# Optimization experiments

Hardware: AMD Instinct MI355X
Metric: run time of the kernel (lower is better)

Reference implementation:

```python
import jax, jax.numpy as jnp
import numpy as np

NUM_HEADS = 8
HEAD_DIM = 64
EMBED = NUM_HEADS * HEAD_DIM  # 512


def setup_inputs() -> dict:
    key = jax.random.key(0)
    ks = jax.random.split(key, 8)
    B, S = 4, 2048
    s = 1.0 / np.sqrt(HEAD_DIM)
    so = 1.0 / np.sqrt(EMBED)
    return {
        "queries": jax.random.normal(ks[0], (B, S, EMBED), jnp.float32),
        "keys": jax.random.normal(ks[1], (B, S, EMBED), jnp.float32),
        "values": jax.random.normal(ks[2], (B, S, EMBED), jnp.float32),
        "Wq": jax.random.uniform(ks[3], (HEAD_DIM, HEAD_DIM), jnp.float32, -s, s),
        "Wk": jax.random.uniform(ks[4], (HEAD_DIM, HEAD_DIM), jnp.float32, -s, s),
        "Wv": jax.random.uniform(ks[5], (HEAD_DIM, HEAD_DIM), jnp.float32, -s, s),
        "Wo": jax.random.uniform(ks[6], (EMBED, EMBED), jnp.float32, -so, so),
        "bo": jax.random.uniform(ks[7], (EMBED,), jnp.float32, -so, so),
    }


def reference(queries, keys, values, Wq, Wk, Wv, Wo, bo):
    B, Sq, _ = queries.shape
    # Faithful to source: keys/values are (buggily) reshaped from `queries`;
    # with equal seq lens this means k/v come from the queries tensor.
    q = queries.reshape(B, Sq, NUM_HEADS, HEAD_DIM)
    k = q
    v = q
    # per-head linear: torch Linear(x) = x @ W.T
    q = jnp.einsum('bshd,ed->bshe', q, Wq)
    k = jnp.einsum('bshd,ed->bshe', k, Wk)
    v = jnp.einsum('bshd,ed->bshe', v, Wv)
    sim = jnp.einsum('bqhd,bkhd->bhqk', q, k)  # [B,H,Sq,Sk]
    attn = jax.nn.softmax(sim * (1.0 / np.sqrt(HEAD_DIM)), axis=-1)
    out = jnp.einsum('bhqk,bkhd->bqhd', attn, v)
    out = out.reshape(B, Sq, EMBED)
    return out @ Wo.T + bo
```

## Files before the change

### kernel.cpp

```cpp
#include <hip/hip_runtime.h>
#include <cstddef>

#define S_ 2048
#define E_ 512
#define SPLIT_STRIDE 4194304u

typedef __attribute__((ext_vector_type(8)))  short bf16x8;
typedef __attribute__((ext_vector_type(16))) float f32x16;

__device__ __forceinline__ unsigned short f2bf(float f) {
    union { float f; unsigned u; } v; v.f = f;
    return (unsigned short)((v.u + 0x7FFFu + ((v.u >> 16) & 1u)) >> 16);
}
__device__ __forceinline__ unsigned pk2bf(float a, float b) {
    union { float f; unsigned u; } x, y; x.f = a; y.f = b;
    return __builtin_amdgcn_perm(y.u + 0x8000u, x.u + 0x8000u, 0x07060302u);
}
__device__ __forceinline__ float bflo(unsigned u) {
    union { unsigned u; float f; } v; v.u = u << 16; return v.f;
}
__device__ __forceinline__ float bfhi(unsigned u) {
    union { unsigned u; float f; } v; v.u = u & 0xffff0000u; return v.f;
}
__device__ __forceinline__ float fexp2(float x) {
#if __has_builtin(__builtin_amdgcn_exp2f)
    return __builtin_amdgcn_exp2f(x);
#else
    return exp2f(x);
#endif
}

__global__ __launch_bounds__(256) void prep_all(const float* __restrict__ X,
                                                const float* __restrict__ Wq,
                                                const float* __restrict__ Wk,
                                                const float* __restrict__ Wo,
                                                const float* __restrict__ Wv,
                                                unsigned short* __restrict__ Xbf,
                                                unsigned short* __restrict__ XTg,
                                                unsigned short* __restrict__ GT,
                                                unsigned short* __restrict__ W2) {
    __shared__ unsigned short T[64][72];
    const int bi = blockIdx.x, tid = threadIdx.x;
    if (bi < 1024) {
        const int st = bi & 31, h = (bi >> 5) & 7, b = bi >> 8;
        const int s0 = st * 64;
        const int j = tid >> 2, g = tid & 3;
        const float* src = X + ((size_t)(b * S_ + s0 + j) * E_) + h * 64 + g * 16;
        unsigned short us[16];
#pragma unroll
        for (int i = 0; i < 16; i += 4) {
            float4 f = *(const float4*)(src + i);
            us[i] = f2bf(f.x); us[i + 1] = f2bf(f.y);
            us[i + 2] = f2bf(f.z); us[i + 3] = f2bf(f.w);
        }
        size_t xb = ((size_t)(b * S_ + s0 + j) * E_) + h * 64 + g * 16;
        *(uint4*)&Xbf[xb]     = *(uint4*)&us[0];
        *(uint4*)&Xbf[xb + 8] = *(uint4*)&us[8];
#pragma unroll
        for (int i = 0; i < 16; ++i) T[g * 16 + i][j] = us[i];
        __syncthreads();
        const int d = tid >> 2;
        const int pm[16] = {0,1,2,3,8,9,10,11,4,5,6,7,12,13,14,15};
        unsigned short o[16];
#pragma unroll
        for (int i = 0; i < 16; ++i) o[i] = T[d][g * 16 + pm[i]];
        size_t tb = ((size_t)((b * 8 + h) * 64 + d)) * S_ + s0 + g * 16;
        *(uint4*)&XTg[tb]     = *(uint4*)&o[0];
        *(uint4*)&XTg[tb + 8] = *(uint4*)&o[8];
    } else if (bi < 1040) {
        int idx = (bi - 1024) * 256 + tid;
        int c = idx >> 6, d = idx & 63;
        float acc = 0.f;
#pragma unroll 8
        for (int e = 0; e < 64; ++e) acc += Wq[e * 64 + d] * Wk[e * 64 + c];
        GT[c * 64 + d] = f2bf(acc * 0.18033688011112042f);
    } else {
        int idx = (bi - 1040) * 256 + tid;
        int e = idx >> 9, f = idx & 511;
        int h = f >> 6, c = f & 63;
        const float* wo = Wo + e * 512 + h * 64;
        float acc = 0.f;
#pragma unroll 8
        for (int d = 0; d < 64; ++d) acc += wo[d] * Wv[d * 64 + c];
        W2[idx] = f2bf(acc);
    }
}

__global__ __launch_bounds__(128, 2) void attn_mfma(const unsigned short* __restrict__ Xbf,
                                                    const unsigned short* __restrict__ XTg,
                                                    const unsigned short* __restrict__ GT,
                                                    unsigned short* __restrict__ AOp,
                                                    float* __restrict__ Lp) {
    __shared__ union SM {
        unsigned short Q[128][72];
        unsigned short cbuf[2][2 * 64 * 72];
        unsigned short AOt[128][72];
    } sm;

    const int tid = threadIdx.x;
    const int w = tid >> 6, lane = tid & 63;
    const int lm = lane & 31, lh = lane >> 5;
    const int h = blockIdx.x & 7;
    const int rest = blockIdx.x >> 3;
    const int qt = rest & 15, b = (rest >> 4) & 3, split = rest >> 6;
    const int s0 = qt * 128, sk0 = split * (S_ / 2);

    {
        const int r = tid >> 1, c = (tid & 1) * 32;
#pragma unroll
        for (int p = 0; p < 2; ++p) {
            const unsigned short* src = Xbf + ((size_t)(b * S_ + s0 + 64 * p + r)) * E_ + h * 64 + c;
#pragma unroll
            for (int u = 0; u < 4; ++u)
                *(uint4*)&sm.Q[64 * p + r][c + u * 8] = *(const uint4*)(src + u * 8);
        }
    }
    __syncthreads();

    const int rr = tid >> 1, cc = (tid & 1) * 32;
    const unsigned short* srcX = Xbf + ((size_t)(b * S_ + rr)) * E_ + h * 64 + cc;
    const unsigned short* srcT = XTg + ((size_t)((b * 8 + h) * 64 + rr)) * S_ + cc;
    const int ldsOff = rr * 72 + cc;

    uint4 pre[8];
    {
        const unsigned short* sx = srcX + (size_t)sk0 * E_;
        const unsigned short* st = srcT + sk0;
#pragma unroll
        for (int u = 0; u < 4; ++u) pre[u]     = *(const uint4*)(sx + u * 8);
#pragma unroll
        for (int u = 0; u < 4; ++u) pre[4 + u] = *(const uint4*)(st + u * 8);
    }

    bf16x8 Ufrag[2][4];
    {
        f32x16 ua[2][2];
#pragma unroll
        for (int mt = 0; mt < 2; ++mt)
#pragma unroll
            for (int nt = 0; nt < 2; ++nt)
#pragma unroll
                for (int i = 0; i < 16; ++i) ua[mt][nt][i] = 0.f;
#pragma unroll
        for (int ks = 0; ks < 4; ++ks) {
            bf16x8 bG0 = *(const bf16x8*)&GT[(lm +  0) * 64 + ks * 16 + lh * 8];
            bf16x8 bG1 = *(const bf16x8*)&GT[(lm + 32) * 64 + ks * 16 + lh * 8];
#pragma unroll
            for (int mt = 0; mt < 2; ++mt) {
                bf16x8 aQ = *(const bf16x8*)&sm.Q[64 * w + 32 * mt + lm][ks * 16 + lh * 8];
                ua[mt][0] = __builtin_amdgcn_mfma_f32_32x32x16_bf16(aQ, bG0, ua[mt][0], 0, 0, 0);
                ua[mt][1] = __builtin_amdgcn_mfma_f32_32x32x16_bf16(aQ, bG1, ua[mt][1], 0, 0, 0);
            }
        }
#pragma unroll
        for (int mt = 0; mt < 2; ++mt)
#pragma unroll
            for (int nt = 0; nt < 2; ++nt)
#pragma unroll
                for (int r = 0; r < 16; ++r)
                    sm.Q[64 * w + 32 * mt + (r & 3) + 8 * (r >> 2) + 4 * lh][lm + 32 * nt] =
                        f2bf(ua[mt][nt][r]);
#pragma unroll
        for (int g = 0; g < 2; ++g)
#pragma unroll
            for (int ks = 0; ks < 4; ++ks)
                Ufrag[g][ks] = *(const bf16x8*)&sm.Q[64 * w + 32 * g + lm][ks * 16 + lh * 8];
    }
    __syncthreads();

    unsigned short* bufR = sm.cbuf[0];
    unsigned short* bufW = sm.cbuf[1];

    {
#pragma unroll
        for (int u = 0; u < 4; ++u) *(uint4*)(bufR + ldsOff + u * 8)           = pre[u];
#pragma unroll
        for (int u = 0; u < 4; ++u) *(uint4*)(bufR + 64 * 72 + ldsOff + u * 8) = pre[4 + u];
    }
    __syncthreads();

    float lsum0 = 0.f, lsum1 = 0.f;
    f32x16 AO[2][2];
#pragma unroll
    for (int mt = 0; mt < 2; ++mt)
#pragma unroll
        for (int nt = 0; nt < 2; ++nt)
#pragma unroll
            for (int i = 0; i < 16; ++i) AO[mt][nt][i] = 0.f;

    for (int ck = 0; ck < 16; ++ck) {
        const bool have = (ck < 15);
        if (have) {
            const unsigned short* sx = srcX + (size_t)(sk0 + (ck + 1) * 64) * E_;
            const unsigned short* st = srcT + sk0 + (ck + 1) * 64;
#pragma unroll
            for (int u = 0; u < 4; ++u) pre[u]     = *(const uint4*)(sx + u * 8);
#pragma unroll
            for (int u = 0; u < 4; ++u) pre[4 + u] = *(const uint4*)(st + u * 8);
        }

        f32x16 sc[2][2];
#pragma unroll
        for (int mt = 0; mt < 2; ++mt)
#pragma unroll
            for (int nt = 0; nt < 2; ++nt)
#pragma unroll
                for (int i = 0; i < 16; ++i) sc[mt][nt][i] = 0.f;
        __builtin_amdgcn_s_setprio(1);
#pragma unroll
        for (int ks = 0; ks < 4; ++ks)
#pragma unroll
            for (int mt = 0; mt < 2; ++mt) {
                bf16x8 aX = *(const bf16x8*)(bufR + (32 * mt + lm) * 72 + ks * 16 + lh * 8);
                sc[mt][0] = __builtin_amdgcn_mfma_f32_32x32x16_bf16(aX, Ufrag[0][ks], sc[mt][0], 0, 0, 0);
                sc[mt][1] = __builtin_amdgcn_mfma_f32_32x32x16_bf16(aX, Ufrag[1][ks], sc[mt][1], 0, 0, 0);
            }
        __builtin_amdgcn_s_setprio(0);

#pragma unroll
        for (int js = 0; js < 4; ++js) {
            const int mt = js >> 1;
            union { unsigned u[4]; bf16x8 v; } bP0, bP1;
#pragma unroll
            for (int i = 0; i < 4; ++i) {
                const int qq = 2 * (js & 1) + (i >> 1);
                float pa = fexp2(sc[mt][0][qq * 4 + 2 * (i & 1)]);
                float pb = fexp2(sc[mt][0][qq * 4 + 2 * (i & 1) + 1]);
                lsum0 += pa + pb;
                bP0.u[i] = pk2bf(pa, pb);
                float pc = fexp2(sc[mt][1][qq * 4 + 2 * (i & 1)]);
                float pd = fexp2(sc[mt][1][qq * 4 + 2 * (i & 1) + 1]);
                lsum1 += pc + pd;
                bP1.u[i] = pk2bf(pc, pd);
            }
            __builtin_amdgcn_s_setprio(1);
#pragma unroll
            for (int mtv = 0; mtv < 2; ++mtv) {
                bf16x8 aT = *(const bf16x8*)(bufR + 64 * 72 + (32 * mtv + lm) * 72 + js * 16 + lh * 8);
                AO[mtv][0] = __builtin_amdgcn_mfma_f32_32x32x16_bf16(aT, bP0.v, AO[mtv][0], 0, 0, 0);
                AO[mtv][1] = __builtin_amdgcn_mfma_f32_32x32x16_bf16(aT, bP1.v, AO[mtv][1], 0, 0, 0);
            }
            __builtin_amdgcn_s_setprio(0);
        }

        if (have) {
#pragma unroll
            for (int u = 0; u < 4; ++u) *(uint4*)(bufW + ldsOff + u * 8)           = pre[u];
#pragma unroll
            for (int u = 0; u < 4; ++u) *(uint4*)(bufW + 64 * 72 + ldsOff + u * 8) = pre[4 + u];
        }
        __syncthreads();
        unsigned short* t = bufR; bufR = bufW; bufW = t;
    }

    lsum0 += __shfl_xor(lsum0, 32);
    lsum1 += __shfl_xor(lsum1, 32);
#pragma unroll
    for (int mtv = 0; mtv < 2; ++mtv)
#pragma unroll
        for (int nt = 0; nt < 2; ++nt)
#pragma unroll
            for (int qq = 0; qq < 4; ++qq) {
                const int d0 = 32 * mtv + 8 * qq + 4 * lh;
                const int row = 64 * w + 32 * nt + lm;
                *(unsigned*)&sm.AOt[row][d0] =
                    pk2bf(AO[mtv][nt][qq * 4 + 0], AO[mtv][nt][qq * 4 + 1]);
                *(unsigned*)&sm.AOt[row][d0 + 2] =
                    pk2bf(AO[mtv][nt][qq * 4 + 2], AO[mtv][nt][qq * 4 + 3]);
            }
    __syncthreads();
    {
        const int r = tid >> 1, c = (tid & 1) * 32;
#pragma unroll
        for (int p = 0; p < 2; ++p) {
            unsigned short* dst = AOp + (size_t)split * SPLIT_STRIDE
                                + ((size_t)(b * S_ + s0 + 64 * p + r)) * E_ + h * 64 + c;
#pragma unroll
            for (int u = 0; u < 4; ++u)
                *(uint4*)(dst + u * 8) = *(const uint4*)&sm.AOt[64 * p + r][c + u * 8];
        }
    }
    if (lane < 32) {
        const size_t lb = ((size_t)(split * 4 + b) * 8 + h) * S_ + s0 + 64 * w;
        Lp[lb + lm]      = lsum0;
        Lp[lb + 32 + lm] = lsum1;
    }
}

__global__ __launch_bounds__(256) void out_gemm_bf(const unsigned short* __restrict__ AOp,
                                                   const float* __restrict__ Lp,
                                                   const unsigned short* __restrict__ W2,
                                                   const float* __restrict__ bo,
                                                   float* __restrict__ out) {
    __shared__ unsigned short At[64][72];
    __shared__ unsigned short Bt[64][72];
    const int tid = threadIdx.x;
    const int w = tid >> 6, lane = tid & 63;
    const int lm = lane & 31, lh = lane >> 5;
    const int et = blockIdx.x & 7, rt = blockIdx.x >> 3;
    const int r0 = rt * 64, e0 = et * 64;
    const int rr = tid >> 2, cc = (tid & 3) * 16;
    const int srow = r0 + rr, bb = srow >> 11, ss = srow & 2047;

    f32x16 acc;
#pragma unroll
    for (int i = 0; i < 16; ++i) acc[i] = 0.f;

    for (int k0 = 0; k0 < 512; k0 += 64) {
        const int hh = k0 >> 6;
        const float linv = 1.0f / (Lp[((size_t)(bb)*8 + hh) * S_ + ss] +
                                   Lp[((size_t)(4 + bb) * 8 + hh) * S_ + ss]);
        __syncthreads();
        {
            const unsigned short* a0 = AOp + (size_t)srow * 512 + k0 + cc;
            const unsigned short* a1 = a0 + SPLIT_STRIDE;
            uint4 u0 = *(const uint4*)a0, u0b = *(const uint4*)(a0 + 8);
            uint4 u1 = *(const uint4*)a1, u1b = *(const uint4*)(a1 + 8);
            uint4 o, ob;
            o.x  = pk2bf((bflo(u0.x) + bflo(u1.x)) * linv, (bfhi(u0.x) + bfhi(u1.x)) * linv);
            o.y  = pk2bf((bflo(u0.y) + bflo(u1.y)) * linv, (bfhi(u0.y) + bfhi(u1.y)) * linv);
            o.z  = pk2bf((bflo(u0.z) + bflo(u1.z)) * linv, (bfhi(u0.z) + bfhi(u1.z)) * linv);
            o.w  = pk2bf((bflo(u0.w) + bflo(u1.w)) * linv, (bfhi(u0.w) + bfhi(u1.w)) * linv);
            ob.x = pk2bf((bflo(u0b.x) + bflo(u1b.x)) * linv, (bfhi(u0b.x) + bfhi(u1b.x)) * linv);
            ob.y = pk2bf((bflo(u0b.y) + bflo(u1b.y)) * linv, (bfhi(u0b.y) + bfhi(u1b.y)) * linv);
            ob.z = pk2bf((bflo(u0b.z) + bflo(u1b.z)) * linv, (bfhi(u0b.z) + bfhi(u1b.z)) * linv);
            ob.w = pk2bf((bflo(u0b.w) + bflo(u1b.w)) * linv, (bfhi(u0b.w) + bfhi(u1b.w)) * linv);
            *(uint4*)&At[rr][cc]     = o;
            *(uint4*)&At[rr][cc + 8] = ob;
            const unsigned short* sb = W2 + (size_t)(e0 + rr) * 512 + k0 + cc;
            *(uint4*)&Bt[rr][cc]     = *(const uint4*)sb;
            *(uint4*)&Bt[rr][cc + 8] = *(const uint4*)(sb + 8);
        }
        __syncthreads();
#pragma unroll
        for (int ks = 0; ks < 4; ++ks) {
            bf16x8 aA = *(const bf16x8*)&At[32 * (w & 1) + lm][ks * 16 + lh * 8];
            bf16x8 bW = *(const bf16x8*)&Bt[32 * (w >> 1) + lm][ks * 16 + lh * 8];
            acc = __builtin_amdgcn_mfma_f32_32x32x16_bf16(aA, bW, acc, 0, 0, 0);
        }
    }
    const float bv = bo[e0 + 32 * (w >> 1) + lm];
#pragma unroll
    for (int r = 0; r < 16; ++r) {
        int orow = r0 + 32 * (w & 1) + (r & 3) + 8 * (r >> 2) + 4 * lh;
        out[(size_t)orow * 512 + e0 + 32 * (w >> 1) + lm] = acc[r] + bv;
    }
}

extern "C" void kernel_launch(void* const* d_in, const int* in_sizes, int n_in,
                              void* d_out, int out_size, void* d_ws, size_t ws_size,
                              hipStream_t stream) {
    (void)in_sizes; (void)n_in; (void)out_size; (void)ws_size;
    const float* X  = (const float*)d_in[0];
    const float* Wq = (const float*)d_in[3];
    const float* Wk = (const float*)d_in[4];
    const float* Wv = (const float*)d_in[5];
    const float* Wo = (const float*)d_in[6];
    const float* bo = (const float*)d_in[7];

    float* ws = (float*)d_ws;
    unsigned short* W2bf = (unsigned short*)ws;
    unsigned short* GT   = (unsigned short*)(ws + 131072);
    unsigned short* Xbf  = (unsigned short*)(ws + 133120);
    unsigned short* XTg  = (unsigned short*)(ws + 2230272);
    unsigned short* AOp  = (unsigned short*)(ws + 4327424);
    float*          Lp   = ws + 8521728;

    prep_all   <<<2064, 256, 0, stream>>>(X, Wq, Wk, Wo, Wv, Xbf, XTg, GT, W2bf);
    attn_mfma  <<<1024, 128, 0, stream>>>(Xbf, XTg, GT, AOp, Lp);
    out_gemm_bf<<<1024, 256, 0, stream>>>(AOp, Lp, W2bf, bo, (float*)d_out);
}
```

Before: 200.9 us.

## Stream K/V chunks via global_load_lds into XOR-swizzled LDS buffers

```diff
diff --git a/kernel.cpp b/kernel.cpp
--- a/kernel.cpp
+++ b/kernel.cpp
@@ -93,7 +93,7 @@
                                                     float* __restrict__ Lp) {
     __shared__ union SM {
         unsigned short Q[128][72];
-        unsigned short cbuf[2][2 * 64 * 72];
+        unsigned char  cb[2][2][8192];
         unsigned short AOt[128][72];
     } sm;
 
@@ -117,21 +117,6 @@
     }
     __syncthreads();
 
-    const int rr = tid >> 1, cc = (tid & 1) * 32;
-    const unsigned short* srcX = Xbf + ((size_t)(b * S_ + rr)) * E_ + h * 64 + cc;
-    const unsigned short* srcT = XTg + ((size_t)((b * 8 + h) * 64 + rr)) * S_ + cc;
-    const int ldsOff = rr * 72 + cc;
-
-    uint4 pre[8];
-    {
-        const unsigned short* sx = srcX + (size_t)sk0 * E_;
-        const unsigned short* st = srcT + sk0;
-#pragma unroll
-        for (int u = 0; u < 4; ++u) pre[u]     = *(const uint4*)(sx + u * 8);
-#pragma unroll
-        for (int u = 0; u < 4; ++u) pre[4 + u] = *(const uint4*)(st + u * 8);
-    }
-
     bf16x8 Ufrag[2][4];
     {
         f32x16 ua[2][2];
@@ -168,14 +153,17 @@
     }
     __syncthreads();
 
-    unsigned short* bufR = sm.cbuf[0];
-    unsigned short* bufW = sm.cbuf[1];
-
-    {
-#pragma unroll
-        for (int u = 0; u < 4; ++u) *(uint4*)(bufR + ldsOff + u * 8)           = pre[u];
-#pragma unroll
-        for (int u = 0; u < 4; ++u) *(uint4*)(bufR + 64 * 72 + ldsOff + u * 8) = pre[4 + u];
+    const int il = lane >> 3;
+    const int swc = ((lane & 7) ^ (il & 7)) * 8;
+    const unsigned short* gX0 = Xbf + ((size_t)(b * S_ + sk0 + 32 * w + il)) * E_ + h * 64 + swc;
+    const unsigned short* gT0 = XTg + ((size_t)((b * 8 + h) * 64 + 32 * w + il)) * S_ + sk0 + swc;
+
+#pragma unroll
+    for (int i8 = 0; i8 < 4; ++i8) {
+        __builtin_amdgcn_global_load_lds((const unsigned*)(gX0 + (size_t)i8 * 8 * E_),
+                                         (unsigned*)&sm.cb[0][0][(4 * w + i8) * 1024], 16, 0, 0);
+        __builtin_amdgcn_global_load_lds((const unsigned*)(gT0 + (size_t)i8 * 8 * S_),
+                                         (unsigned*)&sm.cb[0][1][(4 * w + i8) * 1024], 16, 0, 0);
     }
     __syncthreads();
 
@@ -188,69 +176,67 @@
 #pragma unroll
             for (int i = 0; i < 16; ++i) AO[mt][nt][i] = 0.f;
 
+    const int xorr = (lm & 7) << 4;
+
     for (int ck = 0; ck < 16; ++ck) {
-        const bool have = (ck < 15);
-        if (have) {
-            const unsigned short* sx = srcX + (size_t)(sk0 + (ck + 1) * 64) * E_;
-            const unsigned short* st = srcT + sk0 + (ck + 1) * 64;
-#pragma unroll
-            for (int u = 0; u < 4; ++u) pre[u]     = *(const uint4*)(sx + u * 8);
-#pragma unroll
-            for (int u = 0; u < 4; ++u) pre[4 + u] = *(const uint4*)(st + u * 8);
-        }
-
-        f32x16 sc[2][2];
-#pragma unroll
-        for (int mt = 0; mt < 2; ++mt)
-#pragma unroll
-            for (int nt = 0; nt < 2; ++nt)
-#pragma unroll
-                for (int i = 0; i < 16; ++i) sc[mt][nt][i] = 0.f;
-        __builtin_amdgcn_s_setprio(1);
-#pragma unroll
-        for (int ks = 0; ks < 4; ++ks)
-#pragma unroll
-            for (int mt = 0; mt < 2; ++mt) {
-                bf16x8 aX = *(const bf16x8*)(bufR + (32 * mt + lm) * 72 + ks * 16 + lh * 8);
-                sc[mt][0] = __builtin_amdgcn_mfma_f32_32x32x16_bf16(aX, Ufrag[0][ks], sc[mt][0], 0, 0, 0);
-                sc[mt][1] = __builtin_amdgcn_mfma_f32_32x32x16_bf16(aX, Ufrag[1][ks], sc[mt][1], 0, 0, 0);
-            }
-        __builtin_amdgcn_s_setprio(0);
-
-#pragma unroll
-        for (int js = 0; js < 4; ++js) {
-            const int mt = js >> 1;
-            union { unsigned u[4]; bf16x8 v; } bP0, bP1;
-#pragma unroll
-            for (int i = 0; i < 4; ++i) {
-                const int qq = 2 * (js & 1) + (i >> 1);
-                float pa = fexp2(sc[mt][0][qq * 4 + 2 * (i & 1)]);
-                float pb = fexp2(sc[mt][0][qq * 4 + 2 * (i & 1) + 1]);
-                lsum0 += pa + pb;
-                bP0.u[i] = pk2bf(pa, pb);
-                float pc = fexp2(sc[mt][1][qq * 4 + 2 * (i & 1)]);
-                float pd = fexp2(sc[mt][1][qq * 4 + 2 * (i & 1) + 1]);
-                lsum1 += pc + pd;
-                bP1.u[i] = pk2bf(pc, pd);
-            }
+        const int rb = ck & 1;
+        if (ck < 15) {
+            const unsigned short* sX = gX0 + (size_t)(ck + 1) * 64 * E_;
+            const unsigned short* sT = gT0 + (ck + 1) * 64;
+            unsigned char* dX = &sm.cb[rb ^ 1][0][4 * w * 1024];
+            unsigned char* dT = &sm.cb[rb ^ 1][1][4 * w * 1024];
+#pragma unroll
+            for (int i8 = 0; i8 < 4; ++i8) {
+                __builtin_amdgcn_global_load_lds((const unsigned*)(sX + (size_t)i8 * 8 * E_),
+                                                 (unsigned*)(dX + i8 * 1024), 16, 0, 0);
+                __builtin_amdgcn_global_load_lds((const unsigned*)(sT + (size_t)i8 * 8 * S_),
+                                                 (unsigned*)(dT + i8 * 1024), 16, 0, 0);
+            }
+        }
+
+        const unsigned char* bX = sm.cb[rb][0];
+        const unsigned char* bT = sm.cb[rb][1];
+
+#pragma unroll
+        for (int mt = 0; mt < 2; ++mt) {
+            f32x16 sv0, sv1;
+#pragma unroll
+            for (int i = 0; i < 16; ++i) { sv0[i] = 0.f; sv1[i] = 0.f; }
             __builtin_amdgcn_s_setprio(1);
 #pragma unroll
-            for (int mtv = 0; mtv < 2; ++mtv) {
-                bf16x8 aT = *(const bf16x8*)(bufR + 64 * 72 + (32 * mtv + lm) * 72 + js * 16 + lh * 8);
-                AO[mtv][0] = __builtin_amdgcn_mfma_f32_32x32x16_bf16(aT, bP0.v, AO[mtv][0], 0, 0, 0);
-                AO[mtv][1] = __builtin_amdgcn_mfma_f32_32x32x16_bf16(aT, bP1.v, AO[mtv][1], 0, 0, 0);
+            for (int ks = 0; ks < 4; ++ks) {
+                bf16x8 aX = *(const bf16x8*)(bX + (32 * mt + lm) * 128 + ((ks * 32 + lh * 16) ^ xorr));
+                sv0 = __builtin_amdgcn_mfma_f32_32x32x16_bf16(aX, Ufrag[0][ks], sv0, 0, 0, 0);
+                sv1 = __builtin_amdgcn_mfma_f32_32x32x16_bf16(aX, Ufrag[1][ks], sv1, 0, 0, 0);
             }
             __builtin_amdgcn_s_setprio(0);
-        }
-
-        if (have) {
-#pragma unroll
-            for (int u = 0; u < 4; ++u) *(uint4*)(bufW + ldsOff + u * 8)           = pre[u];
-#pragma unroll
-            for (int u = 0; u < 4; ++u) *(uint4*)(bufW + 64 * 72 + ldsOff + u * 8) = pre[4 + u];
+#pragma unroll
+            for (int jh = 0; jh < 2; ++jh) {
+                const int js = 2 * mt + jh;
+                union { unsigned u[4]; bf16x8 v; } bP0, bP1;
+#pragma unroll
+                for (int i = 0; i < 4; ++i) {
+                    const int qq = 2 * jh + (i >> 1);
+                    float pa = fexp2(sv0[qq * 4 + 2 * (i & 1)]);
+                    float pb = fexp2(sv0[qq * 4 + 2 * (i & 1) + 1]);
+                    lsum0 += pa + pb;
+                    bP0.u[i] = pk2bf(pa, pb);
+                    float pc = fexp2(sv1[qq * 4 + 2 * (i & 1)]);
+                    float pd = fexp2(sv1[qq * 4 + 2 * (i & 1) + 1]);
+                    lsum1 += pc + pd;
+                    bP1.u[i] = pk2bf(pc, pd);
+                }
+                __builtin_amdgcn_s_setprio(1);
+#pragma unroll
+                for (int mtv = 0; mtv < 2; ++mtv) {
+                    bf16x8 aT = *(const bf16x8*)(bT + (32 * mtv + lm) * 128 + ((js * 32 + lh * 16) ^ xorr));
+                    AO[mtv][0] = __builtin_amdgcn_mfma_f32_32x32x16_bf16(aT, bP0.v, AO[mtv][0], 0, 0, 0);
+                    AO[mtv][1] = __builtin_amdgcn_mfma_f32_32x32x16_bf16(aT, bP1.v, AO[mtv][1], 0, 0, 0);
+                }
+                __builtin_amdgcn_s_setprio(0);
+            }
         }
         __syncthreads();
-        unsigned short* t = bufR; bufR = bufW; bufW = t;
     }
 
     lsum0 += __shfl_xor(lsum0, 32);
```

New measurement: 168.2 us. 1.19x faster.
